# Kernel tuning notes

Measured on AMD Instinct MI355X. Metric: run time of the kernel, lower is better.

## Reference

```python
import jax, jax.numpy as jnp
import numpy as np

B, S, E, H = 4, 1024, 1024, 32
D = E // H  # head_dim == num_heads (required by phase broadcast in original code)


def setup_inputs() -> dict:
    key = jax.random.key(0)
    ks = jax.random.split(key, 20)
    s = 0.02
    inp = {
        "x": jax.random.normal(ks[0], (B, S, E), jnp.float32),
        # q/k/v projections (torch Linear: y = x @ W.T + b)
        "q_w": jax.random.normal(ks[1], (E, E), jnp.float32) * s,
        "q_b": jnp.zeros((E,), jnp.float32),
        "k_w": jax.random.normal(ks[2], (E, E), jnp.float32) * s,
        "k_b": jnp.zeros((E,), jnp.float32),
        "v_w": jax.random.normal(ks[3], (E, E), jnp.float32) * s,
        "v_b": jnp.zeros((E,), jnp.float32),
        # phase encoder: Linear(E,E) -> ReLU -> Linear(E,H)
        "ph_w1": jax.random.normal(ks[4], (E, E), jnp.float32) * s,
        "ph_b1": jnp.zeros((E,), jnp.float32),
        "ph_w2": jax.random.normal(ks[5], (H, E), jnp.float32) * s,
        "ph_b2": jnp.zeros((H,), jnp.float32),
        # nn.MultiheadAttention params (packed in_proj + out_proj)
        "in_proj_w": jax.random.normal(ks[6], (3 * E, E), jnp.float32) * s,
        "in_proj_b": jnp.zeros((3 * E,), jnp.float32),
        "out_proj_w": jax.random.normal(ks[7], (E, E), jnp.float32) * s,
        "out_proj_b": jnp.zeros((E,), jnp.float32),
        # final output projection
        "final_w": jax.random.normal(ks[8], (E, E), jnp.float32) * s,
        "final_b": jnp.zeros((E,), jnp.float32),
    }
    return inp


def _heads(t):  # (B,S,E) -> (B,H,S,D)
    return t.reshape(B, S, H, D).transpose(0, 2, 1, 3)


def _mha(x, in_proj_w, in_proj_b, out_proj_w, out_proj_b):
    # torch nn.MultiheadAttention self-attention, batch_first=True, no mask
    qkv = x @ in_proj_w.T + in_proj_b  # (B,S,3E)
    q, k, v = jnp.split(qkv, 3, axis=-1)
    q, k, v = _heads(q), _heads(k), _heads(v)
    scores = jnp.einsum("bhqd,bhkd->bhqk", q, k) / jnp.sqrt(jnp.float32(D))
    attn = jax.nn.softmax(scores, axis=-1)
    ctx = jnp.einsum("bhqk,bhkd->bhqd", attn, v)
    ctx = ctx.transpose(0, 2, 1, 3).reshape(B, S, E)
    return ctx @ out_proj_w.T + out_proj_b


def reference(x, q_w, q_b, k_w, k_b, v_w, v_b, ph_w1, ph_b1, ph_w2, ph_b2,
              in_proj_w, in_proj_b, out_proj_w, out_proj_b, final_w, final_b):
    Q = _heads(x @ q_w.T + q_b)  # (B,H,S,D)
    K = _heads(x @ k_w.T + k_b)
    V = _heads(x @ v_w.T + v_b)

    # phase: (B,H) -> cos -> broadcast over last (head_dim) axis, D == H
    h = jax.nn.relu(jnp.mean(x, axis=1) @ ph_w1.T + ph_b1)
    phase = jnp.cos(h @ ph_w2.T + ph_b2)  # (B,H)
    phase = phase[:, None, None, :]  # (B,1,1,H) multiplies head_dim axis

    Q = Q * phase
    K = K * phase
    scores = jnp.einsum("bhqd,bhkd->bhqk", Q, K) / jnp.sqrt(jnp.float32(D))
    attn_weights = jax.nn.softmax(scores, axis=-1)  # (B,H,S,S)
    context = jnp.einsum("bhqk,bhkd->bhqd", attn_weights, V)
    context = context.transpose(0, 2, 1, 3).reshape(B, S, E)

    entangled = _mha(context, in_proj_w, in_proj_b, out_proj_w, out_proj_b)
    output = (entangled + context) @ final_w.T + final_b
    return output, attn_weights
```

## Files before the change

kernel.cpp:

```cpp
#include <hip/hip_runtime.h>
#include <hip/hip_bf16.h>
#include <cstdint>
#include <cstddef>

typedef __bf16 bf16_t;
typedef __bf16 bf16x8 __attribute__((ext_vector_type(8)));
typedef __bf16 bf16x4 __attribute__((ext_vector_type(4)));
typedef float  f32x4  __attribute__((ext_vector_type(4)));

static constexpr int Bb = 4, Ss = 1024, Ee = 1024, Hh = 32, Dd = 32;
static constexpr int Ntok = Bb * Ss;
static constexpr int E3   = 3 * Ee;
static constexpr float SCALE2 = 0.25506060570135506f;

__device__ __forceinline__ void gl_lds16(const void* g, void* l) {
  __builtin_amdgcn_global_load_lds(
      (const __attribute__((address_space(1))) void*)g,
      (__attribute__((address_space(3))) void*)l, 16, 0, 0);
}
__device__ __forceinline__ float fexp2(float x) { return __builtin_amdgcn_exp2f(x); }

__global__ __launch_bounds__(256) void conv_all(const float* __restrict__ x,  const float* __restrict__ qw,
                                                const float* __restrict__ kw, const float* __restrict__ vw,
                                                const float* __restrict__ inw,const float* __restrict__ ow,
                                                const float* __restrict__ fw,
                                                bf16_t* xb, bf16_t* qb, bf16_t* kb, bf16_t* vb,
                                                bf16_t* inb, bf16_t* ob, bf16_t* fb) {
  const int i = blockIdx.x * 256 + threadIdx.x;
  const float* src; bf16_t* dst; int base;
  if      (i < 1048576) { src = x;   dst = xb;  base = 0; }
  else if (i < 1310720) { src = qw;  dst = qb;  base = 1048576; }
  else if (i < 1572864) { src = kw;  dst = kb;  base = 1310720; }
  else if (i < 1835008) { src = vw;  dst = vb;  base = 1572864; }
  else if (i < 2621440) { src = inw; dst = inb; base = 1835008; }
  else if (i < 2883584) { src = ow;  dst = ob;  base = 2621440; }
  else                  { src = fw;  dst = fb;  base = 2883584; }
  const int j = i - base;
  const float4 v = *(const float4*)(src + (size_t)j * 4);
  bf16x4 o = {(bf16_t)v.x, (bf16_t)v.y, (bf16_t)v.z, (bf16_t)v.w};
  *(bf16x4*)(dst + (size_t)j * 4) = o;
}

__global__ __launch_bounds__(256) void prepb(const float* __restrict__ qb, const float* __restrict__ kb,
                                             const float* __restrict__ vb, float* __restrict__ o) {
  const int i = blockIdx.x * 256 + threadIdx.x;
  o[i] = (i < 1024) ? qb[i] : (i < 2048) ? kb[i - 1024] : vb[i - 2048];
}

__global__ __launch_bounds__(256) void biasck(const float* __restrict__ fw, const float* __restrict__ ob,
                                              const float* __restrict__ fb, float* __restrict__ bc) {
  const int t = threadIdx.x;
  const int n = blockIdx.x * 64 + (t >> 2), p = t & 3;
  const float* row = fw + (size_t)n * 1024 + p * 256;
  const float* obp = ob + p * 256;
  float s = 0.f;
  for (int j = 0; j < 256; ++j) s += row[j] * obp[j];
  s += __shfl_xor(s, 1);
  s += __shfl_xor(s, 2);
  if (p == 0) bc[n] = s + fb[n];
}

__global__ __launch_bounds__(256) void colmean_part(const float* __restrict__ x,
                                                    float* __restrict__ part) {
  const int b = blockIdx.y, sc = blockIdx.x;
  const float* base = x + ((size_t)b * Ss + sc * 32) * Ee;
  for (int k = 0; k < 4; ++k) {
    const int e = threadIdx.x + k * 256;
    float s = 0.f;
    for (int i = 0; i < 32; ++i) s += base[(size_t)i * Ee + e];
    part[((size_t)sc * 4 + b) * Ee + e] = s;
  }
}
__global__ __launch_bounds__(256) void colmean_fin(const float* __restrict__ part,
                                                   float* __restrict__ xm) {
  const int idx = blockIdx.x * 256 + threadIdx.x;
  const int b = idx >> 10, e = idx & 1023;
  float s = 0.f;
  for (int sc = 0; sc < 32; ++sc) s += part[((size_t)sc * 4 + b) * Ee + e];
  xm[idx] = s * (1.0f / 1024.0f);
}

__global__ __launch_bounds__(256) void hgemm(const float* __restrict__ xm,
                                             const float* __restrict__ w1,
                                             const float* __restrict__ b1,
                                             float* __restrict__ hout) {
  __shared__ float xl[4 * 1024];
  for (int i = threadIdx.x; i < 4096; i += 256) xl[i] = xm[i];
  __syncthreads();
  const int j = blockIdx.x * 64 + (threadIdx.x >> 2);
  const int b = threadIdx.x & 3;
  const float* wr = w1 + (size_t)j * Ee;
  const float* xr = xl + b * 1024;
  float s = 0.f;
  for (int e = 0; e < 1024; ++e) s += xr[e] * wr[e];
  s += b1[j];
  hout[b * 1024 + j] = fmaxf(s, 0.f);
}

__global__ __launch_bounds__(128) void phasek(const float* __restrict__ hin,
                                              const float* __restrict__ w2,
                                              const float* __restrict__ b2,
                                              float* __restrict__ ph) {
  const int t = threadIdx.x;
  const int b = t >> 5, hh = t & 31;
  const float* hr = hin + b * 1024;
  const float* wr = w2 + (size_t)hh * Ee;
  float s = 0.f;
  for (int j = 0; j < 1024; ++j) s += hr[j] * wr[j];
  ph[t] = cosf(s + b2[hh]);
}

__global__ __launch_bounds__(256) void transpose1024(const bf16_t* __restrict__ in,
                                                     bf16_t* __restrict__ out) {
  __shared__ bf16_t t[64][72];
  const int jt = threadIdx.x >> 2, k16 = (threadIdx.x & 3) * 16;
  const int r0 = blockIdx.y * 64, c0 = blockIdx.x * 64;
  const bf16x8 a = *(const bf16x8*)(in + (size_t)(r0 + jt) * 1024 + c0 + k16);
  const bf16x8 b = *(const bf16x8*)(in + (size_t)(r0 + jt) * 1024 + c0 + k16 + 8);
  *(bf16x8*)&t[jt][k16] = a;
  *(bf16x8*)&t[jt][k16 + 8] = b;
  __syncthreads();
  bf16x8 v0, v1;
#pragma unroll
  for (int m = 0; m < 8; ++m) v0[m] = t[k16 + m][jt];
#pragma unroll
  for (int m = 0; m < 8; ++m) v1[m] = t[k16 + 8 + m][jt];
  *(bf16x8*)(out + (size_t)(c0 + jt) * 1024 + r0 + k16) = v0;
  *(bf16x8*)(out + (size_t)(c0 + jt) * 1024 + r0 + k16 + 8) = v1;
}

template <int MODE>
__global__ __launch_bounds__(256) void gemm_bt(const bf16_t* __restrict__ A,
                                               const bf16_t* __restrict__ A2,
                                               const bf16_t* __restrict__ Bt,
                                               const bf16_t* __restrict__ Bt2,
                                               const float* __restrict__ bias,
                                               void* __restrict__ Cout,
                                               const float* __restrict__ phase,
                                               int K, int lda, int ldb, int ldc) {
  __shared__ bf16_t As[128 * 32];
  __shared__ bf16_t Bs[128 * 32];
  const int tid = threadIdx.x;
  const int w = tid >> 6, lane = tid & 63;
  const int nwg = gridDim.x * gridDim.y;
  int flat = blockIdx.y * gridDim.x + blockIdx.x;
  flat = (flat & 7) * (nwg >> 3) + (flat >> 3);
  const int m0 = (flat / gridDim.x) * 128, n0 = (flat % gridDim.x) * 128;
  const int wr = (w >> 1) * 64, wc = (w & 1) * 64;
  const int r_ld = lane >> 2, c_ld = (lane & 3) * 8;
  const int rr = lane & 15, kk8 = (lane >> 4) * 8;
  f32x4 acc[4][4];
#pragma unroll
  for (int m = 0; m < 4; ++m)
#pragma unroll
    for (int n = 0; n < 4; ++n) acc[m][n] = f32x4{0.f, 0.f, 0.f, 0.f};

  for (int kt = 0; kt < K; kt += 32) {
    const bf16_t* Ak = A;
    const bf16_t* Bk = Bt;
    int kk = kt;
    if constexpr (MODE == 5) {
      if (kt >= 1024) { Ak = A2; Bk = Bt2; kk = kt - 1024; }
    }
#pragma unroll
    for (int j = 0; j < 2; ++j) {
      const int r0 = w * 16 + j * 64;
      gl_lds16(Ak + (size_t)(m0 + r0 + r_ld) * lda + kk + c_ld, &As[r0 * 32]);
      gl_lds16(Bk + (size_t)(n0 + r0 + r_ld) * ldb + kk + c_ld, &Bs[r0 * 32]);
    }
    __syncthreads();
    bf16x8 af[4], bfr[4];
#pragma unroll
    for (int m = 0; m < 4; ++m) af[m] = *(const bf16x8*)&As[(wr + m * 16 + rr) * 32 + kk8];
#pragma unroll
    for (int n = 0; n < 4; ++n) bfr[n] = *(const bf16x8*)&Bs[(wc + n * 16 + rr) * 32 + kk8];
#pragma unroll
    for (int m = 0; m < 4; ++m)
#pragma unroll
      for (int n = 0; n < 4; ++n)
        acc[m][n] = __builtin_amdgcn_mfma_f32_16x16x32_bf16(af[m], bfr[n], acc[m][n], 0, 0, 0);
    __syncthreads();
  }

  const int rr4 = (lane >> 4) * 4, cc = lane & 15;
#pragma unroll
  for (int m = 0; m < 4; ++m) {
#pragma unroll
    for (int n = 0; n < 4; ++n) {
      const int gr0 = m0 + wr + m * 16 + rr4;
      const int gc = n0 + wc + n * 16 + cc;
      const float bb = bias ? bias[gc] : 0.f;
#pragma unroll
      for (int i = 0; i < 4; ++i) {
        const size_t idx = (size_t)(gr0 + i) * ldc + gc;
        float v = acc[m][n][i] + bb;
        if constexpr (MODE == 4) {
          if (gc < 2048) v *= phase[(((gr0 + i) >> 10) << 5) + ((gc >> 5) & 31)];
        }
        if constexpr (MODE == 5) ((float*)Cout)[idx] = v;
        else ((bf16_t*)Cout)[idx] = (bf16_t)v;
      }
    }
  }
}

__global__ __launch_bounds__(256) void transpose_v(const bf16_t* __restrict__ src, int rs,
                                                   bf16_t* __restrict__ dst) {
  __shared__ bf16_t buf[128 * 33];
  const int bh = blockIdx.y, b = bh >> 5, h = bh & 31;
  const int s0 = blockIdx.x * 128;
  const bf16_t* in = src + ((size_t)b * Ss + s0) * rs + h * 32;
  for (int e = threadIdx.x; e < 128 * 32; e += 256) {
    const int s = e >> 5, d = e & 31;
    buf[s * 33 + d] = in[(size_t)s * rs + d];
  }
  __syncthreads();
  bf16_t* out = dst + (size_t)bh * (Dd * Ss) + s0;
  for (int e = threadIdx.x; e < 128 * 32; e += 256) {
    const int d = e >> 7, s = e & 127;
    out[(size_t)d * Ss + s] = buf[s * 33 + d];
  }
}

static constexpr int K_PLANE_B = 16400;
static constexpr int V_OFF_B   = 4 * K_PLANE_B;
static constexpr int V_ROW_B   = 2064;
static constexpr int P_OFF_B   = V_OFF_B + 32 * V_ROW_B;
static constexpr int P_WAVE_B  = 2304;
static constexpr int ATTN_LDS  = P_OFF_B + 8 * P_WAVE_B;

template <int WRITE_P>
__global__ __launch_bounds__(512) void attn_fused(const bf16_t* __restrict__ Qm,
                                                  const bf16_t* __restrict__ Km, int rs,
                                                  const bf16_t* __restrict__ Vt,
                                                  float* __restrict__ Pout,
                                                  bf16_t* __restrict__ ctx, float scale2) {
  extern __shared__ char smem[];
  char* Kl = smem;
  char* Vl = smem + V_OFF_B;
  const int tid = threadIdx.x, lane = tid & 63, w = tid >> 6;
  const int g = lane >> 4, r = lane & 15;
  int flat = blockIdx.y * 8 + blockIdx.x;
  flat = (flat & 7) * 128 + (flat >> 3);
  const int bh = flat >> 3, xb = flat & 7;
  const int b = bh >> 5, h = bh & 31;
  char* myP = smem + P_OFF_B + w * P_WAVE_B;

  {
    const bf16_t* Kbase = Km + (size_t)b * Ss * rs + h * 32;
    const int pg = w >> 1, hh = w & 1;
#pragma unroll
    for (int c = 0; c < 8; ++c) {
      const int row0 = hh * 512 + c * 64;
      gl_lds16(Kbase + (size_t)(row0 + lane) * rs + pg * 8, Kl + pg * K_PLANE_B + row0 * 16);
    }
  }
  {
    const bf16_t* vsrc = Vt + (size_t)bh * (Dd * Ss);
#pragma unroll
    for (int rr2 = 0; rr2 < 4; ++rr2) {
      const int row = w * 4 + rr2;
#pragma unroll
      for (int c = 0; c < 2; ++c)
        gl_lds16(vsrc + (size_t)row * Ss + c * 512 + lane * 8, Vl + row * V_ROW_B + c * 1024);
    }
  }
  const int qrow0 = xb * 128 + w * 16;
  const bf16x8 qraw = *(const bf16x8*)(Qm + ((size_t)b * Ss + qrow0 + r) * rs + h * 32 + g * 8);
  bf16x8 qf;
#pragma unroll
  for (int i = 0; i < 8; ++i) qf[i] = (bf16_t)((float)qraw[i] * scale2);
  __syncthreads();

  const f32x4 zero = {0.f, 0.f, 0.f, 0.f};
  float lsum = 0.f, rinv = 1.f;

  if constexpr (WRITE_P) {
    for (int kt = 0; kt < 16; ++kt) {
#pragma unroll
      for (int n = 0; n < 4; ++n) {
        const int key = kt * 64 + n * 16 + r;
        const bf16x8 kf = *(const bf16x8*)(Kl + g * K_PLANE_B + key * 16);
        const f32x4 s = __builtin_amdgcn_mfma_f32_16x16x32_bf16(kf, qf, zero, 0, 0, 0);
#pragma unroll
        for (int i = 0; i < 4; ++i) lsum += fexp2(s[i]);
      }
    }
    lsum += __shfl_xor(lsum, 16);
    lsum += __shfl_xor(lsum, 32);
    rinv = 1.0f / lsum;
  }

  f32x4 acc2[2] = {zero, zero};
  const size_t pbase = (size_t)bh * Ss * Ss;

  for (int kt = 0; kt < 16; ++kt) {
    float p[4][4];
#pragma unroll
    for (int n = 0; n < 4; ++n) {
      const int key = kt * 64 + n * 16 + r;
      const bf16x8 kf = *(const bf16x8*)(Kl + g * K_PLANE_B + key * 16);
      const f32x4 s = __builtin_amdgcn_mfma_f32_16x16x32_bf16(kf, qf, zero, 0, 0, 0);
#pragma unroll
      for (int i = 0; i < 4; ++i) {
        float e = fexp2(s[i]);
        if constexpr (WRITE_P) e *= rinv;
        else lsum += e;
        p[n][i] = e;
      }
      bf16x4 pw = {(bf16_t)p[n][0], (bf16_t)p[n][1], (bf16_t)p[n][2], (bf16_t)p[n][3]};
      *(bf16x4*)(myP + r * 144 + (n * 16 + g * 4) * 2) = pw;
      if constexpr (WRITE_P) {
        f32x4 w4 = {p[n][0], p[n][1], p[n][2], p[n][3]};
        *(f32x4*)&Pout[pbase + (size_t)(qrow0 + r) * Ss + kt * 64 + n * 16 + 4 * g] = w4;
      }
    }
#pragma unroll
    for (int c = 0; c < 2; ++c) {
      const bf16x8 pa = *(const bf16x8*)(myP + r * 144 + (c * 32 + 8 * g) * 2);
#pragma unroll
      for (int dn = 0; dn < 2; ++dn) {
        const bf16x8 vf = *(const bf16x8*)(Vl + (dn * 16 + r) * V_ROW_B +
                                           (kt * 64 + c * 32 + g * 8) * 2);
        acc2[dn] = __builtin_amdgcn_mfma_f32_16x16x32_bf16(vf, pa, acc2[dn], 0, 0, 0);
      }
    }
  }

  if constexpr (!WRITE_P) {
    lsum += __shfl_xor(lsum, 16);
    lsum += __shfl_xor(lsum, 32);
    rinv = 1.0f / lsum;
#pragma unroll
    for (int dn = 0; dn < 2; ++dn)
#pragma unroll
      for (int i = 0; i < 4; ++i) acc2[dn][i] *= rinv;
  }

  float* Ct = (float*)myP;
#pragma unroll
  for (int dn = 0; dn < 2; ++dn)
#pragma unroll
    for (int i = 0; i < 4; ++i)
      Ct[r * 36 + dn * 16 + 4 * g + i] = acc2[dn][i];
  const int q2 = lane >> 2, pt = lane & 3;
  const f32x4 ca = *(const f32x4*)(myP + q2 * 144 + pt * 32);
  const f32x4 cb = *(const f32x4*)(myP + q2 * 144 + pt * 32 + 16);
  bf16x8 cv = {(bf16_t)ca[0], (bf16_t)ca[1], (bf16_t)ca[2], (bf16_t)ca[3],
               (bf16_t)cb[0], (bf16_t)cb[1], (bf16_t)cb[2], (bf16_t)cb[3]};
  *(bf16x8*)&ctx[((size_t)b * Ss + qrow0 + q2) * Ee + h * 32 + pt * 8] = cv;
}

extern "C" void kernel_launch(void* const* d_in, const int* in_sizes, int n_in,
                              void* d_out, int out_size, void* d_ws, size_t ws_size,
                              hipStream_t stream) {
  const float* x     = (const float*)d_in[0];
  const float* q_w   = (const float*)d_in[1];
  const float* q_b   = (const float*)d_in[2];
  const float* k_w   = (const float*)d_in[3];
  const float* k_b   = (const float*)d_in[4];
  const float* v_w   = (const float*)d_in[5];
  const float* v_b   = (const float*)d_in[6];
  const float* ph_w1 = (const float*)d_in[7];
  const float* ph_b1 = (const float*)d_in[8];
  const float* ph_w2 = (const float*)d_in[9];
  const float* ph_b2 = (const float*)d_in[10];
  const float* in_w  = (const float*)d_in[11];
  const float* in_b  = (const float*)d_in[12];
  const float* out_w = (const float*)d_in[13];
  const float* out_b = (const float*)d_in[14];
  const float* fin_w = (const float*)d_in[15];
  const float* fin_b = (const float*)d_in[16];

  float* outp = (float*)d_out;
  float* attn_out = outp + (size_t)Ntok * Ee;

  char* ws = (char*)d_ws;
  size_t off = 0;
  auto alloc = [&](size_t bytes) -> void* {
    void* p = ws + off;
    off += (bytes + 255) & ~(size_t)255;
    return p;
  };
  bf16_t* x_bf  = (bf16_t*)alloc((size_t)Ntok * Ee * 2);
  bf16_t* wqkv  = (bf16_t*)alloc((size_t)E3 * Ee * 2);
  bf16_t* win   = (bf16_t*)alloc((size_t)E3 * Ee * 2);
  bf16_t* wout  = (bf16_t*)alloc((size_t)Ee * Ee * 2);
  bf16_t* wfin  = (bf16_t*)alloc((size_t)Ee * Ee * 2);
  bf16_t* woutT = (bf16_t*)alloc((size_t)Ee * Ee * 2);
  bf16_t* Wc    = (bf16_t*)alloc((size_t)Ee * Ee * 2);
  bf16_t* QKVb  = (bf16_t*)alloc((size_t)Ntok * E3 * 2);
  bf16_t* Vt    = (bf16_t*)alloc((size_t)Bb * Hh * Dd * Ss * 2);
  bf16_t* ctx   = (bf16_t*)alloc((size_t)Ntok * Ee * 2);
  bf16_t* qkv2  = (bf16_t*)alloc((size_t)Ntok * E3 * 2);
  bf16_t* v2t   = (bf16_t*)alloc((size_t)Bb * Hh * Dd * Ss * 2);
  bf16_t* ctx2  = (bf16_t*)alloc((size_t)Ntok * Ee * 2);
  float* part   = (float*)alloc((size_t)32 * 4 * 1024 * 4);
  float* xmean  = (float*)alloc(4096 * 4);
  float* hb     = (float*)alloc(4096 * 4);
  float* phase  = (float*)alloc(128 * 4);
  float* qkvb   = (float*)alloc(3072 * 4);
  float* bias_c = (float*)alloc(1024 * 4);

  hipFuncSetAttribute((const void*)attn_fused<1>,
                      hipFuncAttributeMaxDynamicSharedMemorySize, ATTN_LDS);
  hipFuncSetAttribute((const void*)attn_fused<0>,
                      hipFuncAttributeMaxDynamicSharedMemorySize, ATTN_LDS);

  conv_all<<<12288, 256, 0, stream>>>(x, q_w, k_w, v_w, in_w, out_w, fin_w,
                                      x_bf, wqkv, wqkv + (size_t)Ee * Ee,
                                      wqkv + (size_t)2 * Ee * Ee, win, wout, wfin);
  prepb<<<12, 256, 0, stream>>>(q_b, k_b, v_b, qkvb);
  biasck<<<16, 256, 0, stream>>>(fin_w, out_b, fin_b, bias_c);

  colmean_part<<<dim3(32, 4), 256, 0, stream>>>(x, part);
  colmean_fin<<<16, 256, 0, stream>>>(part, xmean);
  hgemm<<<16, 256, 0, stream>>>(xmean, ph_w1, ph_b1, hb);
  phasek<<<1, 128, 0, stream>>>(hb, ph_w2, ph_b2, phase);

  transpose1024<<<dim3(16, 16), 256, 0, stream>>>(wout, woutT);
  gemm_bt<0><<<dim3(8, 8), 256, 0, stream>>>(wfin, nullptr, woutT, nullptr, nullptr,
                                             Wc, nullptr, 1024, Ee, Ee, Ee);

  gemm_bt<4><<<dim3(24, 32), 256, 0, stream>>>(x_bf, nullptr, wqkv, nullptr, qkvb,
                                               QKVb, phase, 1024, Ee, Ee, E3);
  transpose_v<<<dim3(8, 128), 256, 0, stream>>>(QKVb + 2048, E3, Vt);

  attn_fused<1><<<dim3(8, 128), 512, ATTN_LDS, stream>>>(QKVb, QKVb + 1024, E3, Vt,
                                                         attn_out, ctx, SCALE2);

  gemm_bt<0><<<dim3(24, 32), 256, 0, stream>>>(ctx, nullptr, win, nullptr, in_b,
                                               qkv2, nullptr, 1024, Ee, Ee, E3);
  transpose_v<<<dim3(8, 128), 256, 0, stream>>>(qkv2 + 2048, E3, v2t);
  attn_fused<0><<<dim3(8, 128), 512, ATTN_LDS, stream>>>(qkv2, qkv2 + 1024, E3, v2t,
                                                         nullptr, ctx2, SCALE2);

  gemm_bt<5><<<dim3(8, 32), 256, 0, stream>>>(ctx2, ctx, Wc, wfin, bias_c,
                                              outp, nullptr, 2048, Ee, Ee, Ee);
}
```

Baseline: 518.4 us.

## Use 256x256 pipelined GEMM kernel for QKV projections

Adds a gemm256 kernel with 256x256 tiles, 8 waves and 128KB of LDS. It double-buffers K-slices with direct global-to-LDS loads, uses swizzled LDS addressing, and sets barriers, waitcnt and priority by hand so MFMA work overlaps loads. This kernel replaces the 128x128 gemm_bt for the two 4096x3072 QKV projections, and the phase-multiply epilogue moves into it. The bigger tiles aim to cut global traffic per FLOP and hide memory latency. The cost is one workgroup per CU and a grid of 192 blocks, which may leave some of the 256 CUs idle.

After: 526.0 us. Within noise of the previous version (+1.5%).

```diff
diff --git a/kernel.cpp b/kernel.cpp
--- a/kernel.cpp
+++ b/kernel.cpp
@@ -136,7 +136,6 @@
                                                const bf16_t* __restrict__ Bt2,
                                                const float* __restrict__ bias,
                                                void* __restrict__ Cout,
-                                               const float* __restrict__ phase,
                                                int K, int lda, int ldb, int ldc) {
   __shared__ bf16_t As[128 * 32];
   __shared__ bf16_t Bs[128 * 32];
@@ -194,11 +193,115 @@
       for (int i = 0; i < 4; ++i) {
         const size_t idx = (size_t)(gr0 + i) * ldc + gc;
         float v = acc[m][n][i] + bb;
-        if constexpr (MODE == 4) {
-          if (gc < 2048) v *= phase[(((gr0 + i) >> 10) << 5) + ((gc >> 5) & 31)];
-        }
         if constexpr (MODE == 5) ((float*)Cout)[idx] = v;
         else ((bf16_t*)Cout)[idx] = (bf16_t)v;
+      }
+    }
+  }
+}
+
+static constexpr int G256_LDS = 131072;
+
+#define GPHASE(BUF, KS, FH, STAGE, VM) do {                                             \
+    bf16x8 afr[4], bfr[4];                                                              \
+    {  char* sA = slice(BUF, 0, KS);                                                    \
+       char* sB = slice(BUF, 1, KS);                                                    \
+      _Pragma("unroll") for (int mi = 0; mi < 4; ++mi)                                  \
+        afr[mi] = *(const bf16x8*)(sA + (wm * 128 + FH * 64 + mi * 16 + r) * 64 + xg);  \
+      _Pragma("unroll") for (int ni = 0; ni < 4; ++ni)                                  \
+        bfr[ni] = *(const bf16x8*)(sB + (wn * 64 + ni * 16 + r) * 64 + xg); }           \
+    STAGE;                                                                              \
+    __builtin_amdgcn_s_barrier();                                                       \
+    asm volatile("s_waitcnt lgkmcnt(0)" ::: "memory");                                  \
+    __builtin_amdgcn_sched_barrier(0);                                                  \
+    __builtin_amdgcn_s_setprio(1);                                                      \
+    _Pragma("unroll") for (int mi = 0; mi < 4; ++mi)                                    \
+      _Pragma("unroll") for (int ni = 0; ni < 4; ++ni)                                  \
+        acc[FH * 4 + mi][ni] = __builtin_amdgcn_mfma_f32_16x16x32_bf16(                 \
+            afr[mi], bfr[ni], acc[FH * 4 + mi][ni], 0, 0, 0);                           \
+    __builtin_amdgcn_s_setprio(0);                                                      \
+    VM;                                                                                 \
+    __builtin_amdgcn_s_barrier();                                                       \
+    __builtin_amdgcn_sched_barrier(0);                                                  \
+  } while (0)
+
+#define VMC4 asm volatile("s_waitcnt vmcnt(4)" ::: "memory")
+#define VMC0 asm volatile("s_waitcnt vmcnt(0)" ::: "memory")
+
+template <int MODE>
+__global__ __launch_bounds__(512, 1) void gemm256(const bf16_t* __restrict__ A,
+                                                  const bf16_t* __restrict__ Bt,
+                                                  const float* __restrict__ bias,
+                                                  void* __restrict__ Cout,
+                                                  const float* __restrict__ phase,
+                                                  int lda, int ldb, int ldc) {
+  extern __shared__ char sm[];
+  auto slice = [&](int bu, int op, int ks) -> char* {
+    return sm + ((((bu << 1) | op) << 1 | ks) << 14);
+  };
+  const int tid = threadIdx.x, lane = tid & 63, w = tid >> 6;
+  const int g = lane >> 4, r = lane & 15;
+  const int wm = w >> 2, wn = w & 3;
+  const int xg = ((g ^ (r & 3)) << 4);
+  const int nwg = gridDim.x * gridDim.y;
+  int flat = blockIdx.y * gridDim.x + blockIdx.x;
+  flat = (flat & 7) * (nwg >> 3) + (flat >> 3);
+  const int m0 = (flat / gridDim.x) * 256, n0 = (flat % gridDim.x) * 256;
+
+  auto stage2 = [&](int buf, int op, int ks, int T) {
+    const bf16_t* src = op ? Bt : A;
+    const int ld = op ? ldb : lda;
+    const int b0 = op ? n0 : m0;
+    char* dstb = slice(buf, op, ks);
+#pragma unroll
+    for (int hf = 0; hf < 2; ++hf) {
+      const int row = hf * 128 + w * 16 + (lane >> 2);
+      const int si = lane & 3;
+      gl_lds16(src + (size_t)(b0 + row) * ld + T * 64 + ks * 32 + ((si ^ (row & 3)) << 3),
+               dstb + hf * 8192 + w * 1024);
+    }
+  };
+
+  f32x4 acc[8][4];
+#pragma unroll
+  for (int j = 0; j < 8; ++j)
+#pragma unroll
+    for (int n = 0; n < 4; ++n) acc[j][n] = f32x4{0.f, 0.f, 0.f, 0.f};
+
+  stage2(0, 0, 0, 0); stage2(0, 1, 0, 0); stage2(0, 0, 1, 0); stage2(0, 1, 1, 0);
+  stage2(1, 0, 0, 1); stage2(1, 1, 0, 1);
+  VMC4;
+  __builtin_amdgcn_s_barrier();
+  __builtin_amdgcn_sched_barrier(0);
+
+  for (int i = 0; i < 8; ++i) {
+    const int t1 = 2 * i + 1, t2 = 2 * i + 2, t3 = 2 * i + 3;
+    GPHASE(0, 0, 0, { stage2(1, 0, 1, t1); }, );
+    GPHASE(0, 0, 1, { stage2(1, 1, 1, t1); }, );
+    GPHASE(0, 1, 0, { if (i < 7) stage2(0, 0, 0, t2); }, );
+    GPHASE(0, 1, 1, { if (i < 7) stage2(0, 1, 0, t2); },
+           { if (i < 7) { VMC4; } else { VMC0; } });
+    GPHASE(1, 0, 0, { if (i < 7) stage2(0, 0, 1, t2); }, );
+    GPHASE(1, 0, 1, { if (i < 7) stage2(0, 1, 1, t2); }, );
+    GPHASE(1, 1, 0, { if (i < 7) stage2(1, 0, 0, t3); }, );
+    GPHASE(1, 1, 1, { if (i < 7) stage2(1, 1, 0, t3); },
+           { if (i < 7) { VMC4; } });
+  }
+
+#pragma unroll
+  for (int j = 0; j < 8; ++j) {
+#pragma unroll
+    for (int ni = 0; ni < 4; ++ni) {
+      const int gr0 = m0 + wm * 128 + (j >> 2) * 64 + (j & 3) * 16 + g * 4;
+      const int gc = n0 + wn * 64 + ni * 16 + r;
+      const float bb = bias[gc];
+#pragma unroll
+      for (int ii = 0; ii < 4; ++ii) {
+        float v = acc[j][ni][ii] + bb;
+        if constexpr (MODE == 4) {
+          if (gc < 2048) v *= phase[(((gr0 + ii) >> 10) << 5) + ((gc >> 5) & 31)];
+        }
+        ((bf16_t*)Cout)[(size_t)(gr0 + ii) * ldc + gc] = (bf16_t)v;
       }
     }
   }
@@ -406,6 +509,10 @@
                       hipFuncAttributeMaxDynamicSharedMemorySize, ATTN_LDS);
   hipFuncSetAttribute((const void*)attn_fused<0>,
                       hipFuncAttributeMaxDynamicSharedMemorySize, ATTN_LDS);
+  hipFuncSetAttribute((const void*)gemm256<4>,
+                      hipFuncAttributeMaxDynamicSharedMemorySize, G256_LDS);
+  hipFuncSetAttribute((const void*)gemm256<0>,
+                      hipFuncAttributeMaxDynamicSharedMemorySize, G256_LDS);
 
   conv_all<<<12288, 256, 0, stream>>>(x, q_w, k_w, v_w, in_w, out_w, fin_w,
                                       x_bf, wqkv, wqkv + (size_t)Ee * Ee,
@@ -420,21 +527,21 @@
 
   transpose1024<<<dim3(16, 16), 256, 0, stream>>>(wout, woutT);
   gemm_bt<0><<<dim3(8, 8), 256, 0, stream>>>(wfin, nullptr, woutT, nullptr, nullptr,
-                                             Wc, nullptr, 1024, Ee, Ee, Ee);
-
-  gemm_bt<4><<<dim3(24, 32), 256, 0, stream>>>(x_bf, nullptr, wqkv, nullptr, qkvb,
-                                               QKVb, phase, 1024, Ee, Ee, E3);
+                                             Wc, 1024, Ee, Ee, Ee);
+
+  gemm256<4><<<dim3(12, 16), 512, G256_LDS, stream>>>(x_bf, wqkv, qkvb, QKVb, phase,
+                                                      Ee, Ee, E3);
   transpose_v<<<dim3(8, 128), 256, 0, stream>>>(QKVb + 2048, E3, Vt);
 
   attn_fused<1><<<dim3(8, 128), 512, ATTN_LDS, stream>>>(QKVb, QKVb + 1024, E3, Vt,
                                                          attn_out, ctx, SCALE2);
 
-  gemm_bt<0><<<dim3(24, 32), 256, 0, stream>>>(ctx, nullptr, win, nullptr, in_b,
-                                               qkv2, nullptr, 1024, Ee, Ee, E3);
+  gemm256<0><<<dim3(12, 16), 512, G256_LDS, stream>>>(ctx, win, in_b, qkv2, nullptr,
+                                                      Ee, Ee, E3);
   transpose_v<<<dim3(8, 128), 256, 0, stream>>>(qkv2 + 2048, E3, v2t);
   attn_fused<0><<<dim3(8, 128), 512, ATTN_LDS, stream>>>(qkv2, qkv2 + 1024, E3, v2t,
                                                          nullptr, ctx2, SCALE2);
 
   gemm_bt<5><<<dim3(8, 32), 256, 0, stream>>>(ctx2, ctx, Wc, wfin, bias_c,
-                                              outp, nullptr, 2048, Ee, Ee, Ee);
-}
+                                              outp, 2048, Ee, Ee, Ee);
+}
```
